# Optimization experiments

Hardware: AMD Instinct MI355X
Metric: run time of the kernel (lower is better)

The kernel has to match this reference:

```python
import jax, jax.numpy as jnp
import numpy as np
import math

IN_F, OUT_F, NUM_TOKENS = 2048, 2048, 1024

def _make_tokens(num_tokens):
    positions = jnp.linspace(0.0, 1.0, num_tokens)[:, None]          # [T,1]
    freqs = jnp.linspace(1.0, 10.0, 32)[None, :]                     # [1,32]
    angles = positions * freqs * (2.0 * math.pi)                     # [T,32]
    return jnp.concatenate([jnp.sin(angles), jnp.cos(angles)], -1)   # [T,64]

def setup_inputs() -> dict:
    key = jax.random.key(0)
    k = jax.random.split(key, 5)
    x = jax.random.normal(k[0], (4, 4096, IN_F), dtype=jnp.float32)
    tokens = _make_tokens(NUM_TOKENS).astype(jnp.float32)            # [T,64]
    std = 0.02
    # weights stored as [in, out] so y = h @ W
    Wk1 = std * jax.random.normal(k[1], (64, 64), dtype=jnp.float32)
    Wk2 = std * jax.random.normal(k[2], (64, IN_F), dtype=jnp.float32)
    Wv1 = std * jax.random.normal(k[3], (64, 64), dtype=jnp.float32)
    Wv2 = std * jax.random.normal(k[4], (64, OUT_F), dtype=jnp.float32)
    return {"x": x, "tokens": tokens, "Wk1": Wk1, "Wk2": Wk2, "Wv1": Wv1, "Wv2": Wv2}

def reference(x, tokens, Wk1, Wk2, Wv1, Wv2):
    gelu = lambda h: jax.nn.gelu(h, approximate=False)  # torch F.gelu default is exact
    key_tokens = gelu(tokens @ Wk1) @ Wk2                # [T, in_features]
    value_tokens = gelu(tokens @ Wv1) @ Wv2              # [T, out_features]
    sim = jnp.einsum('bsd,td->bst', x, key_tokens)       # [B,S,T]
    T = sim.shape[-1]
    # row-wise scale: * sqrt(T) / sqrt(sum of squares over tokens)
    denom = jnp.sqrt(jnp.sum(sim * sim, axis=-1, keepdims=True))
    weights = gelu(sim * (jnp.sqrt(jnp.asarray(T, sim.dtype)) / denom))
    return jnp.einsum('bst,tf->bsf', weights, value_tokens)  # [B,S,out_features]
```

## Files before the change

kernel.cpp:

```cpp
#include <hip/hip_runtime.h>
#include <hip/hip_bf16.h>
#include <math.h>

typedef __attribute__((ext_vector_type(4))) float f32x4;
typedef __attribute__((ext_vector_type(8))) short bf16x8;
typedef __attribute__((ext_vector_type(4))) unsigned short u16x4;
typedef __attribute__((ext_vector_type(8))) unsigned short u16x8;
typedef __attribute__((ext_vector_type(2))) unsigned int u32x2;

__device__ __forceinline__ unsigned short f2b(float f) {
  unsigned int u = __builtin_bit_cast(unsigned int, f);
  u += 0x7fffu + ((u >> 16) & 1u);
  return (unsigned short)(u >> 16);
}
__device__ __forceinline__ float gelu_exact(float x) {
  return 0.5f * x * (1.0f + erff(x * 0.70710678118654752440f));
}

__global__ void prep(const float* __restrict__ tokens,
                     const float* __restrict__ Wk1, const float* __restrict__ Wv1,
                     const float* __restrict__ Wk2, const float* __restrict__ Wv2,
                     unsigned short* __restrict__ hkb, unsigned short* __restrict__ hvTb,
                     unsigned short* __restrict__ Wk2b, unsigned short* __restrict__ Wv2Tb) {
  const int tid = threadIdx.x;
  const int bx = blockIdx.x;
  if (bx < 256) {
    __shared__ float tok[4][64];
    const int tl = tid >> 6, j = tid & 63;
    const int t0 = bx * 4;
    tok[tl][j] = tokens[(size_t)(t0 + tl) * 64 + j];
    __syncthreads();
    float sk = 0.f, sv = 0.f;
    #pragma unroll 16
    for (int i = 0; i < 64; ++i) {
      float tv = tok[tl][i];
      sk += tv * Wk1[i * 64 + j];
      sv += tv * Wv1[i * 64 + j];
    }
    hkb[(size_t)(t0 + tl) * 64 + j]  = f2b(gelu_exact(sk));
    hvTb[(size_t)j * 1024 + t0 + tl] = f2b(gelu_exact(sv));
  } else if (bx < 272) {
    const int b = bx - 256;
    for (int i = 0; i < 8; ++i) {
      int idx = b * 2048 + i * 256 + tid;
      f32x4 v = ((const f32x4*)Wk2)[idx];
      u16x4 o; o[0] = f2b(v[0]); o[1] = f2b(v[1]); o[2] = f2b(v[2]); o[3] = f2b(v[3]);
      ((u16x4*)Wk2b)[idx] = o;
    }
  } else {
    __shared__ float t[64][65];
    const int f0 = (bx - 272) * 64;
    for (int i = 0; i < 16; ++i) {
      int idx = i * 256 + tid; int r = idx >> 6, c = idx & 63;
      t[r][c] = Wv2[(size_t)r * 2048 + f0 + c];
    }
    __syncthreads();
    for (int i = 0; i < 16; ++i) {
      int idx = i * 256 + tid; int r = idx >> 6, c = idx & 63;
      Wv2Tb[(size_t)(f0 + r) * 64 + c] = f2b(t[c][r]);
    }
  }
}

__global__ __launch_bounds__(256, 2)
void mainK(const float* __restrict__ x,
           const unsigned short* __restrict__ Wk2b,
           const unsigned short* __restrict__ hkb,
           const unsigned short* __restrict__ hvTb,
           const unsigned short* __restrict__ Wv2Tb,
           float* __restrict__ out) {
  __shared__ __align__(16) char smraw[76800];
  unsigned short* As = (unsigned short*)smraw;
  unsigned short* Bs = (unsigned short*)(smraw + 16384);
  float (*red)[4][64][4] = (float(*)[4][64][4])(smraw + 49152);
  unsigned short (*xw16)[72] = (unsigned short(*)[72])(smraw + 57344);
  unsigned short (*Pl)[32][152] = (unsigned short(*)[32][152])smraw;
  float (*redn)[2][16] = (float(*)[2][16])(smraw + 38912);
  float (*redw)[2][4][64][4] = (float(*)[2][4][64][4])(smraw + 39424);
  unsigned short* Ws = (unsigned short*)smraw;
  unsigned short* wvs = (unsigned short*)(smraw + 32768);
  float (*oS)[136] = (float(*)[136])(smraw + 36864);

  const int tid = threadIdx.x, wave = tid >> 6, lane = tid & 63;
  const int lrow = lane & 15, q = lane >> 4;
  const int r0 = blockIdx.x * 32;
  const int tw = wave * 256;

  {
    const int mt = wave & 1, h = wave >> 1;
    f32x4 aR[4]; u16x8 bR[4];
    f32x4 acc[4] = {};

    #pragma unroll
    for (int i = 0; i < 4; ++i) {
      int u4 = (wave * 4 + i) * 4 + (lane >> 4);
      int r = u4 >> 1, ah = u4 & 1;
      aR[i] = *(const f32x4*)&x[(size_t)(r0 + r) * 2048 + ah * 1024 + (lane & 15) * 4];
      int lin = (wave * 4 + i) * 8 + (lane >> 3);
      int t = lin >> 1, bh = lin & 1;
      bR[i] = *(const u16x8*)&Wk2b[(size_t)t * 2048 + bh * 1024 + (lane & 7) * 8];
    }
    #pragma unroll
    for (int i = 0; i < 4; ++i) {
      int u4 = (wave * 4 + i) * 4 + (lane >> 4);
      int r = u4 >> 1, ah = u4 & 1;
      int uu = ((lane & 15) >> 1) ^ (r & 7);
      u16x4 o;
      o[0] = f2b(aR[i][0]); o[1] = f2b(aR[i][1]); o[2] = f2b(aR[i][2]); o[3] = f2b(aR[i][3]);
      *(u16x4*)&As[(r * 2 + ah) * 64 + (uu << 3) + (lane & 1) * 4] = o;
      int lin = (wave * 4 + i) * 8 + (lane >> 3);
      int t = lin >> 1, bh = lin & 1;
      *(u16x8*)&Bs[(t * 2 + bh) * 64 + (((lane & 7) ^ (t & 7)) << 3)] = bR[i];
    }
    __syncthreads();

    #pragma unroll 1
    for (int s = 0; s < 16; ++s) {
      const int cb = s & 1, nb = cb ^ 1;
      const bool pf = (s + 1) < 16;
      if (pf) {
        #pragma unroll
        for (int i = 0; i < 4; ++i) {
          int u4 = (wave * 4 + i) * 4 + (lane >> 4);
          int r = u4 >> 1, ah = u4 & 1;
          aR[i] = *(const f32x4*)&x[(size_t)(r0 + r) * 2048 + ah * 1024 + (s + 1) * 64 + (lane & 15) * 4];
          int lin = (wave * 4 + i) * 8 + (lane >> 3);
          int t = lin >> 1, bh = lin & 1;
          bR[i] = *(const u16x8*)&Wk2b[(size_t)t * 2048 + bh * 1024 + (s + 1) * 64 + (lane & 7) * 8];
        }
      }
      #pragma unroll
      for (int kk = 0; kk < 2; ++kk) {
        const int ar = mt * 16 + lrow;
        bf16x8 af = *(const bf16x8*)&As[cb * 4096 + (ar * 2 + h) * 64 + (((kk * 4 + q) ^ (ar & 7)) << 3)];
        #pragma unroll
        for (int nt = 0; nt < 4; ++nt) {
          const int br = nt * 16 + lrow;
          bf16x8 bf = *(const bf16x8*)&Bs[cb * 8192 + (br * 2 + h) * 64 + (((kk * 4 + q) ^ (br & 7)) << 3)];
          acc[nt] = __builtin_amdgcn_mfma_f32_16x16x32_bf16(af, bf, acc[nt], 0, 0, 0);
        }
      }
      if (pf) {
        #pragma unroll
        for (int i = 0; i < 4; ++i) {
          int u4 = (wave * 4 + i) * 4 + (lane >> 4);
          int r = u4 >> 1, ah = u4 & 1;
          int uu = ((lane & 15) >> 1) ^ (r & 7);
          u16x4 o;
          o[0] = f2b(aR[i][0]); o[1] = f2b(aR[i][1]); o[2] = f2b(aR[i][2]); o[3] = f2b(aR[i][3]);
          *(u16x4*)&As[nb * 4096 + (r * 2 + ah) * 64 + (uu << 3) + (lane & 1) * 4] = o;
          int lin = (wave * 4 + i) * 8 + (lane >> 3);
          int t = lin >> 1, bh = lin & 1;
          *(u16x8*)&Bs[nb * 8192 + (t * 2 + bh) * 64 + (((lane & 7) ^ (t & 7)) << 3)] = bR[i];
        }
      }
      __syncthreads();
    }

    if (h == 1) {
      #pragma unroll
      for (int nt = 0; nt < 4; ++nt) *(f32x4*)&red[mt][nt][lane][0] = acc[nt];
    }
    __syncthreads();
    if (h == 0) {
      #pragma unroll
      for (int nt = 0; nt < 4; ++nt) {
        f32x4 s2 = acc[nt] + *(const f32x4*)&red[mt][nt][lane][0];
        #pragma unroll
        for (int r = 0; r < 4; ++r)
          xw16[mt * 16 + q * 4 + r][nt * 16 + lrow] = f2b(s2[r]);
      }
    }
    __syncthreads();
  }

  {
    bf16x8 xb[2][2];
    #pragma unroll
    for (int mi = 0; mi < 2; ++mi)
      #pragma unroll
      for (int kk = 0; kk < 2; ++kk)
        xb[mi][kk] = *(const bf16x8*)&xw16[mi * 16 + lrow][kk * 32 + q * 8];

    f32x4 acc[16][2] = {};
    #pragma unroll
    for (int t16 = 0; t16 < 16; ++t16)
      #pragma unroll
      for (int kk = 0; kk < 2; ++kk) {
        bf16x8 a = *(const bf16x8*)&hkb[(size_t)(tw + t16 * 16 + lrow) * 64 + kk * 32 + q * 8];
        #pragma unroll
        for (int mi = 0; mi < 2; ++mi)
          acc[t16][mi] = __builtin_amdgcn_mfma_f32_16x16x32_bf16(a, xb[mi][kk], acc[t16][mi], 0, 0, 0);
      }

    float ss[2] = {0.f, 0.f};
    #pragma unroll
    for (int t16 = 0; t16 < 16; ++t16)
      #pragma unroll
      for (int mi = 0; mi < 2; ++mi)
        #pragma unroll
        for (int r = 0; r < 4; ++r)
          ss[mi] += acc[t16][mi][r] * acc[t16][mi][r];
    #pragma unroll
    for (int mi = 0; mi < 2; ++mi) {
      ss[mi] += __shfl_xor(ss[mi], 16, 64);
      ss[mi] += __shfl_xor(ss[mi], 32, 64);
    }
    if (q == 0) { redn[wave][0][lrow] = ss[0]; redn[wave][1][lrow] = ss[1]; }
    __syncthreads();
    float scale[2];
    #pragma unroll
    for (int mi = 0; mi < 2; ++mi) {
      float t = redn[0][mi][lrow] + redn[1][mi][lrow] + redn[2][mi][lrow] + redn[3][mi][lrow];
      scale[mi] = 32.0f * rsqrtf(fmaxf(t, 1e-20f));
    }

    f32x4 wva[2][4] = {};
    #pragma unroll
    for (int c = 0; c < 2; ++c) {
      #pragma unroll
      for (int t8 = 0; t8 < 8; ++t8) {
        const int t16 = c * 8 + t8;
        #pragma unroll
        for (int mi = 0; mi < 2; ++mi) {
          float g0 = gelu_exact(acc[t16][mi][0] * scale[mi]);
          float g1 = gelu_exact(acc[t16][mi][1] * scale[mi]);
          float g2 = gelu_exact(acc[t16][mi][2] * scale[mi]);
          float g3 = gelu_exact(acc[t16][mi][3] * scale[mi]);
          u32x2 pw;
          pw[0] = (unsigned)f2b(g0) | ((unsigned)f2b(g1) << 16);
          pw[1] = (unsigned)f2b(g2) | ((unsigned)f2b(g3) << 16);
          *(u32x2*)&Pl[wave][mi * 16 + lrow][t8 * 16 + q * 4] = pw;
        }
      }
      #pragma unroll
      for (int kc = 0; kc < 4; ++kc) {
        bf16x8 pa0 = *(const bf16x8*)&Pl[wave][lrow][kc * 32 + q * 8];
        bf16x8 pa1 = *(const bf16x8*)&Pl[wave][16 + lrow][kc * 32 + q * 8];
        #pragma unroll
        for (int nt = 0; nt < 4; ++nt) {
          bf16x8 b = *(const bf16x8*)&hvTb[(size_t)(nt * 16 + lrow) * 1024 +
                                           tw + c * 128 + kc * 32 + q * 8];
          wva[0][nt] = __builtin_amdgcn_mfma_f32_16x16x32_bf16(pa0, b, wva[0][nt], 0, 0, 0);
          wva[1][nt] = __builtin_amdgcn_mfma_f32_16x16x32_bf16(pa1, b, wva[1][nt], 0, 0, 0);
        }
      }
    }

    #pragma unroll
    for (int mi = 0; mi < 2; ++mi)
      #pragma unroll
      for (int nt = 0; nt < 4; ++nt)
        *(f32x4*)&redw[wave][mi][nt][lane][0] = wva[mi][nt];
    __syncthreads();
    #pragma unroll
    for (int mi = 0; mi < 2; ++mi) {
      f32x4 s = *(const f32x4*)&redw[0][mi][wave][lane][0];
      s += *(const f32x4*)&redw[1][mi][wave][lane][0];
      s += *(const f32x4*)&redw[2][mi][wave][lane][0];
      s += *(const f32x4*)&redw[3][mi][wave][lane][0];
      #pragma unroll
      for (int r = 0; r < 4; ++r) {
        int m = mi * 16 + q * 4 + r, j = wave * 16 + lrow;
        wvs[m * 64 + (((j >> 3) ^ (m & 7)) << 3) + (j & 7)] = f2b(s[r]);
      }
    }
    __syncthreads();
  }

  {
    u16x8 wR[4];
    #pragma unroll
    for (int i = 0; i < 4; ++i) {
      int lin = (wave * 4 + i) * 64 + lane;
      int frow = lin >> 3, u = lin & 7;
      wR[i] = *(const u16x8*)&Wv2Tb[(size_t)frow * 64 + u * 8];
    }
    #pragma unroll
    for (int i = 0; i < 4; ++i) {
      int lin = (wave * 4 + i) * 64 + lane;
      int frow = lin >> 3, u = lin & 7;
      *(u16x8*)&Ws[frow * 64 + ((u ^ (frow & 7)) << 3)] = wR[i];
    }
    __syncthreads();

    bf16x8 bw[2][2];
    #pragma unroll
    for (int mt = 0; mt < 2; ++mt)
      #pragma unroll
      for (int kk = 0; kk < 2; ++kk) {
        int row = mt * 16 + lrow;
        bw[mt][kk] = *(const bf16x8*)&wvs[row * 64 + (((kk * 4 + q) ^ (row & 7)) << 3)];
      }

    #pragma unroll 1
    for (int fc = 0; fc < 16; ++fc) {
      const int cb = fc & 1, nb = cb ^ 1;
      const bool pf = (fc + 1) < 16;
      if (pf) {
        #pragma unroll
        for (int i = 0; i < 4; ++i) {
          int lin = (wave * 4 + i) * 64 + lane;
          int frow = lin >> 3, u = lin & 7;
          wR[i] = *(const u16x8*)&Wv2Tb[(size_t)((fc + 1) * 128 + frow) * 64 + u * 8];
        }
      }
      #pragma unroll
      for (int ftl = 0; ftl < 2; ++ftl) {
        const int ft = wave * 2 + ftl;
        f32x4 a2[2] = {};
        #pragma unroll
        for (int kk = 0; kk < 2; ++kk) {
          const int frow = ft * 16 + lrow;
          bf16x8 af = *(const bf16x8*)&Ws[cb * 8192 + frow * 64 + (((kk * 4 + q) ^ (frow & 7)) << 3)];
          #pragma unroll
          for (int mt = 0; mt < 2; ++mt)
            a2[mt] = __builtin_amdgcn_mfma_f32_16x16x32_bf16(af, bw[mt][kk], a2[mt], 0, 0, 0);
        }
        #pragma unroll
        for (int mt = 0; mt < 2; ++mt)
          *(f32x4*)&oS[mt * 16 + lrow][ft * 16 + q * 4] = a2[mt];
      }
      if (pf) {
        #pragma unroll
        for (int i = 0; i < 4; ++i) {
          int lin = (wave * 4 + i) * 64 + lane;
          int frow = lin >> 3, u = lin & 7;
          *(u16x8*)&Ws[nb * 8192 + frow * 64 + ((u ^ (frow & 7)) << 3)] = wR[i];
        }
      }
      __syncthreads();
      #pragma unroll
      for (int i = 0; i < 4; ++i) {
        int row = (wave * 4 + i) * 2 + (lane >> 5);
        int c = (lane & 31) * 4;
        f32x4 v = *(const f32x4*)&oS[row][c];
        *(f32x4*)&out[(size_t)(r0 + row) * 2048 + fc * 128 + c] = v;
      }
      __syncthreads();
    }
  }
}

extern "C" void kernel_launch(void* const* d_in, const int* in_sizes, int n_in,
                              void* d_out, int out_size, void* d_ws, size_t ws_size,
                              hipStream_t stream) {
  (void)in_sizes; (void)n_in; (void)out_size; (void)ws_size;
  const float* x      = (const float*)d_in[0];
  const float* tokens = (const float*)d_in[1];
  const float* Wk1    = (const float*)d_in[2];
  const float* Wk2    = (const float*)d_in[3];
  const float* Wv1    = (const float*)d_in[4];
  const float* Wv2    = (const float*)d_in[5];

  char* ws = (char*)d_ws;
  unsigned short* hkb   = (unsigned short*)(ws);
  unsigned short* hvTb  = (unsigned short*)(ws + 131072);
  unsigned short* Wk2b  = (unsigned short*)(ws + 262144);
  unsigned short* Wv2Tb = (unsigned short*)(ws + 524288);

  hipLaunchKernelGGL(prep, dim3(304), dim3(256), 0, stream,
                     tokens, Wk1, Wv1, Wk2, Wv2, hkb, hvTb, Wk2b, Wv2Tb);
  hipLaunchKernelGGL(mainK, dim3(512), dim3(256), 0, stream,
                     x, Wk2b, hkb, hvTb, Wv2Tb, (float*)d_out);
}
```

Before: 75.96 us.

## Deepen prefetch to two stages and double-buffer output staging

In the x·Wk2 loop and the Wv2 output loop, global loads are now issued two iterations ahead. The registers fetched in the previous iteration are written to the next LDS buffer at the top of each iteration, before the MFMAs. The output staging tile oS is double-buffered, which removes the trailing barrier in each output iteration. The aim is to hide global-load latency better and cut synchronisation, at the cost of more LDS use and longer register lifetimes.

```diff
diff --git a/kernel.cpp b/kernel.cpp
--- a/kernel.cpp
+++ b/kernel.cpp
@@ -79,7 +79,7 @@
   float (*redw)[2][4][64][4] = (float(*)[2][4][64][4])(smraw + 39424);
   unsigned short* Ws = (unsigned short*)smraw;
   unsigned short* wvs = (unsigned short*)(smraw + 32768);
-  float (*oS)[136] = (float(*)[136])(smraw + 36864);
+  float (*oS)[32][136] = (float(*)[32][136])(smraw + 36864);
 
   const int tid = threadIdx.x, wave = tid >> 6, lane = tid & 63;
   const int lrow = lane & 15, q = lane >> 4;
@@ -91,44 +91,34 @@
     f32x4 aR[4]; u16x8 bR[4];
     f32x4 acc[4] = {};
 
-    #pragma unroll
-    for (int i = 0; i < 4; ++i) {
-      int u4 = (wave * 4 + i) * 4 + (lane >> 4);
-      int r = u4 >> 1, ah = u4 & 1;
-      aR[i] = *(const f32x4*)&x[(size_t)(r0 + r) * 2048 + ah * 1024 + (lane & 15) * 4];
-      int lin = (wave * 4 + i) * 8 + (lane >> 3);
-      int t = lin >> 1, bh = lin & 1;
-      bR[i] = *(const u16x8*)&Wk2b[(size_t)t * 2048 + bh * 1024 + (lane & 7) * 8];
-    }
-    #pragma unroll
-    for (int i = 0; i < 4; ++i) {
-      int u4 = (wave * 4 + i) * 4 + (lane >> 4);
-      int r = u4 >> 1, ah = u4 & 1;
-      int uu = ((lane & 15) >> 1) ^ (r & 7);
-      u16x4 o;
-      o[0] = f2b(aR[i][0]); o[1] = f2b(aR[i][1]); o[2] = f2b(aR[i][2]); o[3] = f2b(aR[i][3]);
-      *(u16x4*)&As[(r * 2 + ah) * 64 + (uu << 3) + (lane & 1) * 4] = o;
-      int lin = (wave * 4 + i) * 8 + (lane >> 3);
-      int t = lin >> 1, bh = lin & 1;
-      *(u16x8*)&Bs[(t * 2 + bh) * 64 + (((lane & 7) ^ (t & 7)) << 3)] = bR[i];
-    }
+#define P1_LOAD(sidx)                                                                     \
+    do { _Pragma("unroll") for (int i = 0; i < 4; ++i) {                                  \
+      int u4 = (wave * 4 + i) * 4 + (lane >> 4); int rr = u4 >> 1, ah = u4 & 1;           \
+      aR[i] = *(const f32x4*)&x[(size_t)(r0 + rr) * 2048 + ah * 1024 + (sidx) * 64 + (lane & 15) * 4]; \
+      int lin = (wave * 4 + i) * 8 + (lane >> 3); int t = lin >> 1, bh = lin & 1;         \
+      bR[i] = *(const u16x8*)&Wk2b[(size_t)t * 2048 + bh * 1024 + (sidx) * 64 + (lane & 7) * 8]; \
+    } } while (0)
+
+#define P1_WRITE(buf)                                                                     \
+    do { _Pragma("unroll") for (int i = 0; i < 4; ++i) {                                  \
+      int u4 = (wave * 4 + i) * 4 + (lane >> 4); int rr = u4 >> 1, ah = u4 & 1;           \
+      int uu = ((lane & 15) >> 1) ^ (rr & 7); u16x4 o;                                    \
+      o[0] = f2b(aR[i][0]); o[1] = f2b(aR[i][1]); o[2] = f2b(aR[i][2]); o[3] = f2b(aR[i][3]); \
+      *(u16x4*)&As[(buf) * 4096 + (rr * 2 + ah) * 64 + (uu << 3) + (lane & 1) * 4] = o;   \
+      int lin = (wave * 4 + i) * 8 + (lane >> 3); int t = lin >> 1, bh = lin & 1;         \
+      *(u16x8*)&Bs[(buf) * 8192 + (t * 2 + bh) * 64 + (((lane & 7) ^ (t & 7)) << 3)] = bR[i]; \
+    } } while (0)
+
+    P1_LOAD(0);
+    P1_WRITE(0);
+    P1_LOAD(1);
     __syncthreads();
 
     #pragma unroll 1
     for (int s = 0; s < 16; ++s) {
       const int cb = s & 1, nb = cb ^ 1;
-      const bool pf = (s + 1) < 16;
-      if (pf) {
-        #pragma unroll
-        for (int i = 0; i < 4; ++i) {
-          int u4 = (wave * 4 + i) * 4 + (lane >> 4);
-          int r = u4 >> 1, ah = u4 & 1;
-          aR[i] = *(const f32x4*)&x[(size_t)(r0 + r) * 2048 + ah * 1024 + (s + 1) * 64 + (lane & 15) * 4];
-          int lin = (wave * 4 + i) * 8 + (lane >> 3);
-          int t = lin >> 1, bh = lin & 1;
-          bR[i] = *(const u16x8*)&Wk2b[(size_t)t * 2048 + bh * 1024 + (s + 1) * 64 + (lane & 7) * 8];
-        }
-      }
+      if (s + 1 < 16) P1_WRITE(nb);
+      if (s + 2 < 16) P1_LOAD(s + 2);
       #pragma unroll
       for (int kk = 0; kk < 2; ++kk) {
         const int ar = mt * 16 + lrow;
@@ -140,22 +130,10 @@
           acc[nt] = __builtin_amdgcn_mfma_f32_16x16x32_bf16(af, bf, acc[nt], 0, 0, 0);
         }
       }
-      if (pf) {
-        #pragma unroll
-        for (int i = 0; i < 4; ++i) {
-          int u4 = (wave * 4 + i) * 4 + (lane >> 4);
-          int r = u4 >> 1, ah = u4 & 1;
-          int uu = ((lane & 15) >> 1) ^ (r & 7);
-          u16x4 o;
-          o[0] = f2b(aR[i][0]); o[1] = f2b(aR[i][1]); o[2] = f2b(aR[i][2]); o[3] = f2b(aR[i][3]);
-          *(u16x4*)&As[nb * 4096 + (r * 2 + ah) * 64 + (uu << 3) + (lane & 1) * 4] = o;
-          int lin = (wave * 4 + i) * 8 + (lane >> 3);
-          int t = lin >> 1, bh = lin & 1;
-          *(u16x8*)&Bs[nb * 8192 + (t * 2 + bh) * 64 + (((lane & 7) ^ (t & 7)) << 3)] = bR[i];
-        }
-      }
       __syncthreads();
     }
+#undef P1_LOAD
+#undef P1_WRITE
 
     if (h == 1) {
       #pragma unroll
@@ -270,19 +248,21 @@
 
   {
     u16x8 wR[4];
-    #pragma unroll
-    for (int i = 0; i < 4; ++i) {
-      int lin = (wave * 4 + i) * 64 + lane;
-      int frow = lin >> 3, u = lin & 7;
-      wR[i] = *(const u16x8*)&Wv2Tb[(size_t)frow * 64 + u * 8];
-    }
-    #pragma unroll
-    for (int i = 0; i < 4; ++i) {
-      int lin = (wave * 4 + i) * 64 + lane;
-      int frow = lin >> 3, u = lin & 7;
-      *(u16x8*)&Ws[frow * 64 + ((u ^ (frow & 7)) << 3)] = wR[i];
-    }
-    __syncthreads();
+
+#define P3_LOAD(fcx)                                                                      \
+    do { _Pragma("unroll") for (int i = 0; i < 4; ++i) {                                  \
+      int lin = (wave * 4 + i) * 64 + lane; int frow = lin >> 3, u = lin & 7;             \
+      wR[i] = *(const u16x8*)&Wv2Tb[(size_t)((fcx) * 128 + frow) * 64 + u * 8];           \
+    } } while (0)
+#define P3_WRITE(buf)                                                                     \
+    do { _Pragma("unroll") for (int i = 0; i < 4; ++i) {                                  \
+      int lin = (wave * 4 + i) * 64 + lane; int frow = lin >> 3, u = lin & 7;             \
+      *(u16x8*)&Ws[(buf) * 8192 + frow * 64 + ((u ^ (frow & 7)) << 3)] = wR[i];           \
+    } } while (0)
+
+    P3_LOAD(0);
+    P3_WRITE(0);
+    P3_LOAD(1);
 
     bf16x8 bw[2][2];
     #pragma unroll
@@ -292,19 +272,13 @@
         int row = mt * 16 + lrow;
         bw[mt][kk] = *(const bf16x8*)&wvs[row * 64 + (((kk * 4 + q) ^ (row & 7)) << 3)];
       }
+    __syncthreads();
 
     #pragma unroll 1
     for (int fc = 0; fc < 16; ++fc) {
-      const int cb = fc & 1, nb = cb ^ 1;
-      const bool pf = (fc + 1) < 16;
-      if (pf) {
-        #pragma unroll
-        for (int i = 0; i < 4; ++i) {
-          int lin = (wave * 4 + i) * 64 + lane;
-          int frow = lin >> 3, u = lin & 7;
-          wR[i] = *(const u16x8*)&Wv2Tb[(size_t)((fc + 1) * 128 + frow) * 64 + u * 8];
-        }
-      }
+      const int cb = fc & 1, nb = cb ^ 1, ob = fc & 1;
+      if (fc + 1 < 16) P3_WRITE(nb);
+      if (fc + 2 < 16) P3_LOAD(fc + 2);
       #pragma unroll
       for (int ftl = 0; ftl < 2; ++ftl) {
         const int ft = wave * 2 + ftl;
@@ -319,26 +293,19 @@
         }
         #pragma unroll
         for (int mt = 0; mt < 2; ++mt)
-          *(f32x4*)&oS[mt * 16 + lrow][ft * 16 + q * 4] = a2[mt];
-      }
-      if (pf) {
-        #pragma unroll
-        for (int i = 0; i < 4; ++i) {
-          int lin = (wave * 4 + i) * 64 + lane;
-          int frow = lin >> 3, u = lin & 7;
-          *(u16x8*)&Ws[nb * 8192 + frow * 64 + ((u ^ (frow & 7)) << 3)] = wR[i];
-        }
+          *(f32x4*)&oS[ob][mt * 16 + lrow][ft * 16 + q * 4] = a2[mt];
       }
       __syncthreads();
       #pragma unroll
       for (int i = 0; i < 4; ++i) {
         int row = (wave * 4 + i) * 2 + (lane >> 5);
         int c = (lane & 31) * 4;
-        f32x4 v = *(const f32x4*)&oS[row][c];
+        f32x4 v = *(const f32x4*)&oS[ob][row][c];
         *(f32x4*)&out[(size_t)(r0 + row) * 2048 + fc * 128 + c] = v;
       }
-      __syncthreads();
-    }
+    }
+#undef P3_LOAD
+#undef P3_WRITE
   }
 }
 
```

After: 75.77 us. Within noise of the previous version (-0.3%).
